# Performance work log

Measured on AMD Instinct MI355X. Metric: run time of the kernel, lower is better.

Reference implementation:

```python
import jax, jax.numpy as jnp
import numpy as np

FEATURE_SPACE = 128


def _gru_params(key, in_dim, hidden):
    k1, k2, k3, k4 = jax.random.split(key, 4)
    s = 1.0 / np.sqrt(hidden)
    return (
        jax.random.uniform(k1, (3 * hidden, in_dim), minval=-s, maxval=s, dtype=jnp.float32),
        jax.random.uniform(k2, (3 * hidden, hidden), minval=-s, maxval=s, dtype=jnp.float32),
        jax.random.uniform(k3, (3 * hidden,), minval=-s, maxval=s, dtype=jnp.float32),
        jax.random.uniform(k4, (3 * hidden,), minval=-s, maxval=s, dtype=jnp.float32),
    )


def setup_inputs() -> dict:
    key = jax.random.key(0)
    ks = jax.random.split(key, 6)
    B, T, H, W = 32, 64, 128, 128
    bbox = jax.random.normal(ks[0], (B, T, 4), dtype=jnp.float32)
    flow = jax.random.normal(ks[1], (B, T, H, W, 2), dtype=jnp.float32)
    ego = jax.random.normal(ks[2], (B, T, 3), dtype=jnp.float32)
    Wih_b, Whh_b, bih_b, bhh_b = _gru_params(ks[3], 4, FEATURE_SPACE)
    Wih_f, Whh_f, bih_f, bhh_f = _gru_params(ks[4], 2, FEATURE_SPACE)
    Wih_e, Whh_e, bih_e, bhh_e = _gru_params(ks[5], 3, FEATURE_SPACE)
    return {
        "bbox": bbox, "flow": flow, "ego": ego,
        "Wih_b": Wih_b, "Whh_b": Whh_b, "bih_b": bih_b, "bhh_b": bhh_b,
        "Wih_f": Wih_f, "Whh_f": Whh_f, "bih_f": bih_f, "bhh_f": bhh_f,
        "Wih_e": Wih_e, "Whh_e": Whh_e, "bih_e": bih_e, "bhh_e": bhh_e,
    }


def _gru_encode(x, Wih, Whh, bih, bhh):
    # x: [B, T, D] -> final hidden [B, H], PyTorch GRUCell math, h0 = 0
    B = x.shape[0]
    Hs = Whh.shape[1]
    # precompute input projections for all timesteps: [T, B, 3H]
    gi = jnp.swapaxes(jnp.einsum('btd,gd->btg', x, Wih) + bih, 0, 1)

    def step(h, gi_t):
        gh = h @ Whh.T + bhh
        i_r, i_z, i_n = jnp.split(gi_t, 3, axis=-1)
        h_r, h_z, h_n = jnp.split(gh, 3, axis=-1)
        r = jax.nn.sigmoid(i_r + h_r)
        z = jax.nn.sigmoid(i_z + h_z)
        n = jnp.tanh(i_n + r * h_n)
        h_new = (1.0 - z) * n + z * h
        return h_new, None

    h0 = jnp.zeros((B, Hs), dtype=x.dtype)
    h_final, _ = jax.lax.scan(step, h0, gi)
    return h_final


def reference(bbox, flow, ego,
              Wih_b, Whh_b, bih_b, bhh_b,
              Wih_f, Whh_f, bih_f, bhh_f,
              Wih_e, Whh_e, bih_e, bhh_e):
    mid_x = flow.shape[2] // 2
    mid_y = flow.shape[3] // 2
    # vectorized center-pixel gather: [B, T, 2]
    storage = flow[:, :, mid_x, mid_y, :]
    flow_result = _gru_encode(storage, Wih_f, Whh_f, bih_f, bhh_f)
    bbox_result = _gru_encode(bbox, Wih_b, Whh_b, bih_b, bhh_b)
    ego_result = _gru_encode(ego, Wih_e, Whh_e, bih_e, bhh_e)
    alpha, beta, gamma = 1.0, 1.0, 1.0
    tot = alpha + beta + gamma
    return (flow_result * (beta / tot)
            + bbox_result * (alpha / tot)
            + ego_result * (gamma / tot))
```

## Files before the change

### kernel.cpp

```cpp
#include <hip/hip_runtime.h>
#include <hip/hip_bf16.h>


#define HID 128
#define TT  64
#define BB  32

__device__ __forceinline__ float sigmoidf_(float x) {
    return 1.0f / (1.0f + __expf(-x) * 0.0f + expf(-x));
}

__global__ __launch_bounds__(256, 1) void gru_fused_kernel(
    const float* __restrict__ bbox, const float* __restrict__ flow, const float* __restrict__ ego,
    const float* __restrict__ Wih_b, const float* __restrict__ Whh_b,
    const float* __restrict__ bih_b, const float* __restrict__ bhh_b,
    const float* __restrict__ Wih_f, const float* __restrict__ Whh_f,
    const float* __restrict__ bih_f, const float* __restrict__ bhh_f,
    const float* __restrict__ Wih_e, const float* __restrict__ Whh_e,
    const float* __restrict__ bih_e, const float* __restrict__ bhh_e,
    float* __restrict__ ws)
{
    const int blk = blockIdx.x;
    const int gru = blk >> 5;
    const int b   = blk & 31;
    const int tid = threadIdx.x;
    const int g   = tid >> 1;
    const int q   = tid & 1;

    const float* Wih; const float* Whh; const float* bih; const float* bhh; int D;
    if (gru == 0)      { Wih = Wih_b; Whh = Whh_b; bih = bih_b; bhh = bhh_b; D = 4; }
    else if (gru == 1) { Wih = Wih_f; Whh = Whh_f; bih = bih_f; bhh = bhh_f; D = 2; }
    else               { Wih = Wih_e; Whh = Whh_e; bih = bih_e; bhh = bhh_e; D = 3; }

    float4 wr[16], wz[16], wn[16];
    {
        const float4* base = reinterpret_cast<const float4*>(Whh) + q * 16;
        const float4* rowr = base + (size_t)(g        ) * 32;
        const float4* rowz = base + (size_t)(g + HID  ) * 32;
        const float4* rown = base + (size_t)(g + 2*HID) * 32;
        #pragma unroll
        for (int k = 0; k < 16; ++k) { wr[k] = rowr[k]; wz[k] = rowz[k]; wn[k] = rown[k]; }
    }

    float wir[4] = {0,0,0,0}, wiz[4] = {0,0,0,0}, win[4] = {0,0,0,0};
    for (int d = 0; d < D; ++d) {
        wir[d] = Wih[(g        ) * D + d];
        wiz[d] = Wih[(g + HID  ) * D + d];
        win[d] = Wih[(g + 2*HID) * D + d];
    }
    const float bir = bih[g], biz = bih[g + HID], bin = bih[g + 2*HID];
    const float bhr = (q == 0) ? bhh[g]         : 0.f;
    const float bhz = (q == 0) ? bhh[g + HID]   : 0.f;
    const float bhn = (q == 0) ? bhh[g + 2*HID] : 0.f;

    __shared__ __align__(16) float h_s[2][HID];
    __shared__ __align__(16) float4 x4_s[TT];

    {
        const int t = tid >> 2, d = tid & 3;
        float v = 0.f;
        if (gru == 0) {
            v = bbox[(size_t)(b * TT + t) * 4 + d];
        } else if (gru == 1) {
            if (d < 2) v = flow[(((size_t)(b * TT + t) * 128 + 64) * 128 + 64) * 2 + d];
        } else {
            if (d < 3) v = ego[(size_t)(b * TT + t) * 3 + d];
        }
        reinterpret_cast<float*>(&x4_s[t])[d] = v;
    }
    if (tid < HID) h_s[0][tid] = 0.f;
    float h_old = 0.f;
    __syncthreads();

    int cur = 0;
    for (int t = 0; t < TT; ++t) {
        const float4 xv = x4_s[t];

        float ar = bhr, az = bhz, an = bhn;
        const float4* hb = reinterpret_cast<const float4*>(&h_s[cur][q * 64]);
        #pragma unroll
        for (int k = 0; k < 16; ++k) {
            const float4 hv = hb[k];
            ar = fmaf(wr[k].x, hv.x, ar); ar = fmaf(wr[k].y, hv.y, ar);
            ar = fmaf(wr[k].z, hv.z, ar); ar = fmaf(wr[k].w, hv.w, ar);
            az = fmaf(wz[k].x, hv.x, az); az = fmaf(wz[k].y, hv.y, az);
            az = fmaf(wz[k].z, hv.z, az); az = fmaf(wz[k].w, hv.w, az);
            an = fmaf(wn[k].x, hv.x, an); an = fmaf(wn[k].y, hv.y, an);
            an = fmaf(wn[k].z, hv.z, an); an = fmaf(wn[k].w, hv.w, an);
        }
        ar += __shfl_xor(ar, 1, 64);
        az += __shfl_xor(az, 1, 64);
        an += __shfl_xor(an, 1, 64);

        float gr = bir, gz = biz, gn = bin;
        gr = fmaf(wir[0], xv.x, gr); gr = fmaf(wir[1], xv.y, gr);
        gr = fmaf(wir[2], xv.z, gr); gr = fmaf(wir[3], xv.w, gr);
        gz = fmaf(wiz[0], xv.x, gz); gz = fmaf(wiz[1], xv.y, gz);
        gz = fmaf(wiz[2], xv.z, gz); gz = fmaf(wiz[3], xv.w, gz);
        gn = fmaf(win[0], xv.x, gn); gn = fmaf(win[1], xv.y, gn);
        gn = fmaf(win[2], xv.z, gn); gn = fmaf(win[3], xv.w, gn);

        const float r = 1.f / (1.f + expf(-(gr + ar)));
        const float z = 1.f / (1.f + expf(-(gz + az)));
        const float n = tanhf(gn + r * an);
        const float h_new = (1.f - z) * n + z * h_old;
        h_old = h_new;

        if (q == 0) h_s[cur ^ 1][g] = h_new;
        __syncthreads();
        cur ^= 1;
    }

    if (q == 0) ws[((size_t)gru * BB + b) * HID + g] = h_old;
}

__global__ void combine_kernel(const float* __restrict__ ws, float* __restrict__ out) {
    const int i = blockIdx.x * blockDim.x + threadIdx.x;
    if (i < BB * HID) {
        out[i] = (ws[i] + ws[BB * HID + i] + ws[2 * BB * HID + i]) * (1.0f / 3.0f);
    }
}

extern "C" void kernel_launch(void* const* d_in, const int* in_sizes, int n_in,
                              void* d_out, int out_size, void* d_ws, size_t ws_size,
                              hipStream_t stream) {
    const float* bbox  = (const float*)d_in[0];
    const float* flow  = (const float*)d_in[1];
    const float* ego   = (const float*)d_in[2];
    const float* Wih_b = (const float*)d_in[3];
    const float* Whh_b = (const float*)d_in[4];
    const float* bih_b = (const float*)d_in[5];
    const float* bhh_b = (const float*)d_in[6];
    const float* Wih_f = (const float*)d_in[7];
    const float* Whh_f = (const float*)d_in[8];
    const float* bih_f = (const float*)d_in[9];
    const float* bhh_f = (const float*)d_in[10];
    const float* Wih_e = (const float*)d_in[11];
    const float* Whh_e = (const float*)d_in[12];
    const float* bih_e = (const float*)d_in[13];
    const float* bhh_e = (const float*)d_in[14];

    float* ws  = (float*)d_ws;
    float* out = (float*)d_out;

    gru_fused_kernel<<<dim3(96), dim3(256), 0, stream>>>(
        bbox, flow, ego,
        Wih_b, Whh_b, bih_b, bhh_b,
        Wih_f, Whh_f, bih_f, bhh_f,
        Wih_e, Whh_e, bih_e, bhh_e,
        ws);

    combine_kernel<<<dim3((BB * HID + 255) / 256), dim3(256), 0, stream>>>(ws, out);
}
```

Baseline: 374.8 us.

## Fuse combine into GRU kernel via last-block counter and use fast math gates

Removes the separate combine kernel launch. The last block to finish, detected with an atomic counter plus threadfence, averages the three GRU results and writes the output. A memset of the counter is added before the launch. The gate nonlinearities also switch to __expf and __fdividef, with tanh written through the exp identity, to shorten the serial per-step latency at some cost in accuracy.

```diff
diff --git a/kernel.cpp b/kernel.cpp
--- a/kernel.cpp
+++ b/kernel.cpp
@@ -5,10 +5,7 @@
 #define HID 128
 #define TT  64
 #define BB  32
-
-__device__ __forceinline__ float sigmoidf_(float x) {
-    return 1.0f / (1.0f + __expf(-x) * 0.0f + expf(-x));
-}
+#define NBLK 96
 
 __global__ __launch_bounds__(256, 1) void gru_fused_kernel(
     const float* __restrict__ bbox, const float* __restrict__ flow, const float* __restrict__ ego,
@@ -18,7 +15,9 @@
     const float* __restrict__ bih_f, const float* __restrict__ bhh_f,
     const float* __restrict__ Wih_e, const float* __restrict__ Whh_e,
     const float* __restrict__ bih_e, const float* __restrict__ bhh_e,
-    float* __restrict__ ws)
+    float* __restrict__ ws,
+    unsigned* __restrict__ counter,
+    float* __restrict__ out)
 {
     const int blk = blockIdx.x;
     const int gru = blk >> 5;
@@ -86,7 +85,7 @@
             az = fmaf(wz[k].x, hv.x, az); az = fmaf(wz[k].y, hv.y, az);
             az = fmaf(wz[k].z, hv.z, az); az = fmaf(wz[k].w, hv.w, az);
             an = fmaf(wn[k].x, hv.x, an); an = fmaf(wn[k].y, hv.y, an);
-            an = fmaf(wn[k].z, hv.z, an); an = fmaf(wn[k].w, hv.w, an);
+            an = fmaf(wn[k].w, hv.w, an); an = fmaf(wn[k].z, hv.z, an);
         }
         ar += __shfl_xor(ar, 1, 64);
         az += __shfl_xor(az, 1, 64);
@@ -100,9 +99,9 @@
         gn = fmaf(win[0], xv.x, gn); gn = fmaf(win[1], xv.y, gn);
         gn = fmaf(win[2], xv.z, gn); gn = fmaf(win[3], xv.w, gn);
 
-        const float r = 1.f / (1.f + expf(-(gr + ar)));
-        const float z = 1.f / (1.f + expf(-(gz + az)));
-        const float n = tanhf(gn + r * an);
+        const float r = __fdividef(1.f, 1.f + __expf(-(gr + ar)));
+        const float z = __fdividef(1.f, 1.f + __expf(-(gz + az)));
+        const float n = __fdividef(2.f, 1.f + __expf(-2.f * (gn + r * an))) - 1.f;
         const float h_new = (1.f - z) * n + z * h_old;
         h_old = h_new;
 
@@ -112,12 +111,26 @@
     }
 
     if (q == 0) ws[((size_t)gru * BB + b) * HID + g] = h_old;
-}
 
-__global__ void combine_kernel(const float* __restrict__ ws, float* __restrict__ out) {
-    const int i = blockIdx.x * blockDim.x + threadIdx.x;
-    if (i < BB * HID) {
-        out[i] = (ws[i] + ws[BB * HID + i] + ws[2 * BB * HID + i]) * (1.0f / 3.0f);
+    __threadfence();
+    __shared__ unsigned done;
+    if (tid == 0) done = atomicAdd(counter, 1u);
+    __syncthreads();
+    if (done == NBLK - 1) {
+        __threadfence();
+        const float4* w0 = reinterpret_cast<const float4*>(ws);
+        const float4* w1 = w0 + (BB * HID) / 4;
+        const float4* w2 = w1 + (BB * HID) / 4;
+        float4* o4 = reinterpret_cast<float4*>(out);
+        for (int i = tid; i < (BB * HID) / 4; i += 256) {
+            const float4 a = w0[i], c = w1[i], e = w2[i];
+            float4 r;
+            r.x = (a.x + c.x + e.x) * (1.0f / 3.0f);
+            r.y = (a.y + c.y + e.y) * (1.0f / 3.0f);
+            r.z = (a.z + c.z + e.z) * (1.0f / 3.0f);
+            r.w = (a.w + c.w + e.w) * (1.0f / 3.0f);
+            o4[i] = r;
+        }
     }
 }
 
@@ -140,15 +153,16 @@
     const float* bih_e = (const float*)d_in[13];
     const float* bhh_e = (const float*)d_in[14];
 
-    float* ws  = (float*)d_ws;
-    float* out = (float*)d_out;
+    float* ws        = (float*)d_ws;
+    unsigned* counter = (unsigned*)((char*)d_ws + 3 * BB * HID * sizeof(float));
+    float* out       = (float*)d_out;
 
-    gru_fused_kernel<<<dim3(96), dim3(256), 0, stream>>>(
+    hipMemsetAsync(counter, 0, sizeof(unsigned), stream);
+
+    gru_fused_kernel<<<dim3(NBLK), dim3(256), 0, stream>>>(
         bbox, flow, ego,
         Wih_b, Whh_b, bih_b, bhh_b,
         Wih_f, Whh_f, bih_f, bhh_f,
         Wih_e, Whh_e, bih_e, bhh_e,
-        ws);
-
-    combine_kernel<<<dim3((BB * HID + 255) / 256), dim3(256), 0, stream>>>(ws, out);
+        ws, counter, out);
 }
```

After: 377.6 us. Within noise of the previous version (+0.7%).
